# Kernel tuning notes

Hardware: AMD Instinct MI355X
Metric: run time of the kernel (lower is better)

## Reference

```python
import jax, jax.numpy as jnp
import numpy as np

B, S, D, NH = 2, 1024, 2048, 8
QK, V, I = 1024, 2048, 8192  # qk_dim = D/2, v_dim = D, intermediate = 4D
CAP = 15.0
EPS = 1e-6


def setup_inputs() -> dict:
    key = jax.random.key(0)
    ks = jax.random.split(key, 12)
    sc = D ** -0.5
    return {
        "x": jax.random.normal(ks[0], (B, S, D), jnp.float32),
        "Wq": jax.random.normal(ks[1], (D, QK), jnp.float32) * sc,
        "Wk": jax.random.normal(ks[2], (D, QK), jnp.float32) * sc,
        "Wv": jax.random.normal(ks[3], (D, V), jnp.float32) * sc,
        "Wo": jax.random.normal(ks[4], (D, V), jnp.float32) * sc,
        "Wi": jax.random.normal(ks[5], (D, NH), jnp.float32) * sc,
        "bi": -10.0 * jnp.ones((NH,), jnp.float32),   # xLSTM input-gate bias init
        "Wf": jax.random.normal(ks[6], (D, NH), jnp.float32) * sc,
        "bf": jnp.linspace(3.0, 6.0, NH, dtype=jnp.float32),  # forget-gate bias init
        "mh_norm_w": jnp.ones((V,), jnp.float32),
        "Wout": jax.random.normal(ks[7], (V, D), jnp.float32) * (V ** -0.5),
        "rms1_w": jnp.ones((D,), jnp.float32),
        "Wgate": jax.random.normal(ks[8], (D, I), jnp.float32) * sc,
        "Wup": jax.random.normal(ks[9], (D, I), jnp.float32) * sc,
        "Wdown": jax.random.normal(ks[10], (I, D), jnp.float32) * (I ** -0.5),
        "rms2_w": jnp.ones((D,), jnp.float32),
    }


def soft_cap(x, cap=CAP):
    return cap * jnp.tanh(x / cap)


def rms_norm(x, w, eps=EPS):
    xf = x.astype(jnp.float32)
    var = jnp.mean(xf * xf, axis=-1, keepdims=True)
    return (w * (xf * jax.lax.rsqrt(var + eps))).astype(x.dtype)


def mlstm_stabilized(q, k, v, i, f):
    # q,k: [B,NH,S,DQK]; v: [B,NH,S,DV]; i,f: [B,NH,S] (soft-capped preacts)
    dqk = q.shape[-1]
    logf = jax.nn.log_sigmoid(f.astype(jnp.float32))
    lfc = jnp.cumsum(logf, axis=-1)                         # [B,NH,S]
    tri = jnp.tril(jnp.ones((S, S), bool))
    # log decay D[t,s] = sum_{j=s+1..t} log sig(f_j) + i_s  (causal)
    logD = jnp.where(tri, lfc[..., :, None] - lfc[..., None, :], -jnp.inf) + i[..., None, :]
    m = jnp.max(logD, axis=-1, keepdims=True)               # [B,NH,S,1] stabilizer
    Dm = jnp.exp(logD - m)
    scores = jnp.einsum("bhsd,bhtd->bhst", q, k) * (dqk ** -0.5) * Dm
    n = jnp.maximum(jnp.abs(scores.sum(-1, keepdims=True)), jnp.exp(-m))
    return jnp.einsum("bhst,bhtv->bhsv", scores, v) / (n + EPS)  # [B,NH,S,DV]


def xlstm_layer(x, Wq, Wk, Wv, Wo, Wi, bi, Wf, bf, mh_norm_w, Wout):
    q = (x @ Wq).reshape(B, S, NH, -1).transpose(0, 2, 1, 3)
    k = (x @ Wk).reshape(B, S, NH, -1).transpose(0, 2, 1, 3)
    v = (x @ Wv).reshape(B, S, NH, -1).transpose(0, 2, 1, 3)
    o_preact = x @ Wo                                       # [B,S,V]
    i = soft_cap(x @ Wi + bi).transpose(0, 2, 1)            # [B,NH,S]
    f = soft_cap(x @ Wf + bf).transpose(0, 2, 1)
    h = mlstm_stabilized(q, k, v, i, f)                     # [B,NH,S,DV]
    h = h.transpose(0, 2, 1, 3)                             # [B,S,NH,DV]
    # multi-head RMS norm over per-head value dim
    hf = h.astype(jnp.float32)
    var = jnp.mean(hf * hf, axis=-1, keepdims=True)
    hn = (hf * jax.lax.rsqrt(var + EPS)).reshape(B, S, V) * mh_norm_w
    h_out = jax.nn.sigmoid(o_preact) * hn                   # output gate
    return h_out @ Wout


def reference(x, Wq, Wk, Wv, Wo, Wi, bi, Wf, bf, mh_norm_w, Wout, rms1_w,
              Wgate, Wup, Wdown, rms2_w):
    residual = x
    h = xlstm_layer(x, Wq, Wk, Wv, Wo, Wi, bi, Wf, bf, mh_norm_w, Wout)
    h = residual + rms_norm(h, rms1_w)
    mlp = (jax.nn.silu(h @ Wgate) * (h @ Wup)) @ Wdown
    return h + rms_norm(mlp, rms2_w)
```

## Files before the change

kernel.cpp:

```cpp
#include <hip/hip_runtime.h>
#include <hip/hip_bf16.h>

#define TOKENS 2048
#define DMODEL 2048
#define SEQ    1024
#define QKVO   6144

typedef __attribute__((ext_vector_type(8))) short bf16x8;
typedef __attribute__((ext_vector_type(4))) short bf16x4;
typedef __attribute__((ext_vector_type(4))) float f32x4;
typedef __attribute__((ext_vector_type(8))) unsigned short u16x8;
typedef __attribute__((ext_vector_type(4))) unsigned short u16x4;

__device__ __forceinline__ float sigmoidf_(float x) { return 1.f / (1.f + expf(-x)); }
__device__ __forceinline__ float softcapf_(float x) { return 15.f * tanhf(x * (1.f / 15.f)); }
__device__ __forceinline__ float logsigf_(float x) {
  return (x >= 0.f) ? -log1pf(expf(-x)) : (x - log1pf(expf(x)));
}
__device__ __forceinline__ unsigned short f2bf(float f) {
  unsigned u = __builtin_bit_cast(unsigned, f);
  u += 0x7FFFu + ((u >> 16) & 1u);
  return (unsigned short)(u >> 16);
}
__device__ __forceinline__ float bf2f(unsigned short b) {
  unsigned u = ((unsigned)b) << 16;
  return __builtin_bit_cast(float, u);
}

typedef __attribute__((address_space(3))) void lds_void;
typedef const __attribute__((address_space(1))) void gmem_void;
__device__ __forceinline__ void gload16(const void* g, void* l) {
  __builtin_amdgcn_global_load_lds((gmem_void*)g, (lds_void*)l, 16, 0, 0);
}
__device__ __forceinline__ unsigned lds_off(const void* p) {
  return (unsigned)(size_t)(__attribute__((address_space(3))) const void*)p;
}

#if defined(__has_builtin)
#if __has_builtin(__builtin_amdgcn_mfma_f32_16x16x16bf16_1k)
#define HAVE_MFMA16 1
#endif
#endif

__device__ __forceinline__ f32x4 mfma16_bf16(bf16x4 a, bf16x4 b, f32x4 c) {
#ifdef HAVE_MFMA16
  return __builtin_amdgcn_mfma_f32_16x16x16bf16_1k(a, b, c, 0, 0, 0);
#else
  f32x4 d;
  asm volatile("v_mfma_f32_16x16x16_bf16 %0, %1, %2, %3"
               : "=v"(d) : "v"(a), "v"(b), "v"(c));
  return d;
#endif
}

__device__ __forceinline__ bf16x4 tr_read(unsigned addr) {
  bf16x4 d;
  asm volatile("ds_read_b64_tr_b16 %0, %1" : "=v"(d) : "v"(addr));
  return d;
}

__device__ __forceinline__ void remap_block(int& bm, int& bn) {
  const int nbx = gridDim.x, nby = gridDim.y;
  const int bid = blockIdx.y * nbx + blockIdx.x;
  const int q = (nbx * nby) >> 3;
  const int lid = (bid & 7) * q + (bid >> 3);
  bm = lid % nby;
  bn = lid / nby;
}

template <int EPI>
__global__ __launch_bounds__(512) void gemm256(
    const unsigned short* __restrict__ A, const unsigned short* __restrict__ BT,
    void* __restrict__ Cout, const unsigned short* __restrict__ aux,
    int M, int N, int K, int ldk) {
  __shared__ unsigned short lds[3][2][8192];
  const int tid = threadIdx.x;
  int bm, bn;
  remap_block(bm, bn);
  const int m0 = bm * 256, n0 = bn * 256;
  const int wid = tid >> 6, lane = tid & 63;
  const int wr = wid >> 2, wc = wid & 3;
  const int fr = lane & 15, fq = lane >> 4;
  const size_t kz = (size_t)blockIdx.z * K;

  const f32x4 zero = {0.f, 0.f, 0.f, 0.f};
  f32x4 acc[8][4];
#pragma unroll
  for (int m = 0; m < 8; ++m)
#pragma unroll
    for (int n = 0; n < 4; ++n) acc[m][n] = zero;

  const int sr = tid >> 2;
  const int sc = tid & 3;
  const int sgc = sc ^ ((sr + (sr >> 2)) & 3);
  const unsigned short* Asrc = A + kz + (size_t)(m0 + sr) * ldk + sgc * 8;
  const unsigned short* Bsrc = BT + kz + (size_t)(n0 + sr) * ldk + sgc * 8;
  const size_t hstep = (size_t)128 * ldk;
  const int ldst = sr * 32 + sc * 8;

  const int rsw = (fq ^ ((fr + (fr >> 2)) & 3)) * 8;
  const int arow0 = wr * 128 + fr;
  const int brow0 = wc * 64 + fr;

  auto stage = [&](int t) {
    const size_t ko = (size_t)t * 32;
    const int bs = t % 3;
    gload16(Asrc + ko, &lds[bs][0][ldst]);
    gload16(Asrc + ko + hstep, &lds[bs][0][4096 + ldst]);
    gload16(Bsrc + ko, &lds[bs][1][ldst]);
    gload16(Bsrc + ko + hstep, &lds[bs][1][4096 + ldst]);
  };

  const int NT = K >> 5;
  stage(0);
  stage(1);

  for (int t = 0; t < NT; ++t) {
    if (t + 1 < NT) {
      asm volatile("s_waitcnt vmcnt(4)" ::: "memory");
    } else {
      asm volatile("s_waitcnt vmcnt(0)" ::: "memory");
    }
    __builtin_amdgcn_s_barrier();
    if (t + 2 < NT) stage(t + 2);
    const int b = t % 3;
    const unsigned short* la = &lds[b][0][0];
    const unsigned short* lb = &lds[b][1][0];
    bf16x8 bfm[4], af[4];
#pragma unroll
    for (int n = 0; n < 4; ++n)
      bfm[n] = *(const bf16x8*)&lb[(brow0 + n * 16) * 32 + rsw];
#pragma unroll
    for (int m = 0; m < 4; ++m)
      af[m] = *(const bf16x8*)&la[(arow0 + m * 16) * 32 + rsw];
    __builtin_amdgcn_s_setprio(1);
#pragma unroll
    for (int m = 0; m < 4; ++m)
#pragma unroll
      for (int n = 0; n < 4; ++n)
        acc[m][n] = __builtin_amdgcn_mfma_f32_16x16x32_bf16(af[m], bfm[n],
                                                            acc[m][n], 0, 0, 0);
    __builtin_amdgcn_s_setprio(0);
#pragma unroll
    for (int m = 0; m < 4; ++m)
      af[m] = *(const bf16x8*)&la[(arow0 + 64 + m * 16) * 32 + rsw];
    __builtin_amdgcn_s_setprio(1);
#pragma unroll
    for (int m = 0; m < 4; ++m)
#pragma unroll
      for (int n = 0; n < 4; ++n)
        acc[4 + m][n] = __builtin_amdgcn_mfma_f32_16x16x32_bf16(
            af[m], bfm[n], acc[4 + m][n], 0, 0, 0);
    __builtin_amdgcn_s_setprio(0);
  }

  const int orow = m0 + wr * 128 + fq * 4;
  const int ocol = n0 + wc * 64 + fr;
#pragma unroll
  for (int m = 0; m < 8; ++m) {
#pragma unroll
    for (int n = 0; n < 4; ++n) {
      const int cc = ocol + n * 16;
#pragma unroll
      for (int j = 0; j < 4; ++j) {
        const int r = orow + m * 16 + j;
        float v = acc[m][n][j];
        if (EPI == 0) {
          ((float*)Cout + (size_t)blockIdx.z * M * N)[(size_t)r * N + cc] = v;
        } else if (EPI == 1) {
          ((unsigned short*)Cout)[(size_t)r * N + cc] = f2bf(v);
        } else {
          const size_t idx = (size_t)r * N + cc;
          const float gv = bf2f(aux[idx]);
          ((unsigned short*)Cout)[idx] = f2bf(v * gv * sigmoidf_(gv));
        }
      }
    }
  }
}

template <int EPI>
__global__ __launch_bounds__(256) void gemm_bf16(
    const unsigned short* __restrict__ A, const unsigned short* __restrict__ BT,
    void* __restrict__ Cout, int M, int N, int K) {
  __shared__ unsigned short As[2][128 * 32];
  __shared__ unsigned short Bs[2][128 * 32];
  const int tid = threadIdx.x;
  int bm, bn;
  remap_block(bm, bn);
  const int m0 = bm * 128;
  const int n0 = bn * 128;
  const int wid = tid >> 6;
  const int lane = tid & 63;
  const int wr = wid >> 1, wc = wid & 1;
  const int fr = lane & 15, fq = lane >> 4;

  const f32x4 zero = {0.f, 0.f, 0.f, 0.f};
  f32x4 acc[4][4];
#pragma unroll
  for (int m = 0; m < 4; ++m)
#pragma unroll
    for (int n = 0; n < 4; ++n) acc[m][n] = zero;

  const int srow = tid >> 2;
  const int sc = tid & 3;
  const int sgc = sc ^ ((srow + (srow >> 2)) & 3);
  const int scol = sgc * 8;
  const unsigned short* Ag0 = A + (size_t)(m0 + srow) * K + scol;
  const unsigned short* Ag1 = A + (size_t)(m0 + 64 + srow) * K + scol;
  const unsigned short* Bg0 = BT + (size_t)(n0 + srow) * K + scol;
  const unsigned short* Bg1 = BT + (size_t)(n0 + 64 + srow) * K + scol;
  const int rsw = (fq ^ ((fr + (fr >> 2)) & 3)) * 8;

  gload16(Ag0, &As[0][tid * 8]);
  gload16(Ag1, &As[0][2048 + tid * 8]);
  gload16(Bg0, &Bs[0][tid * 8]);
  gload16(Bg1, &Bs[0][2048 + tid * 8]);
  __syncthreads();

  const int nt = K >> 5;
  for (int t = 0; t < nt; ++t) {
    const int cur = t & 1;
    if (t + 1 < nt) {
      const int k0 = (t + 1) << 5;
      gload16(Ag0 + k0, &As[cur ^ 1][tid * 8]);
      gload16(Ag1 + k0, &As[cur ^ 1][2048 + tid * 8]);
      gload16(Bg0 + k0, &Bs[cur ^ 1][tid * 8]);
      gload16(Bg1 + k0, &Bs[cur ^ 1][2048 + tid * 8]);
    }
    bf16x8 af[4], bfm[4];
#pragma unroll
    for (int m = 0; m < 4; ++m)
      af[m] = *(const bf16x8*)&As[cur][(wr * 64 + m * 16 + fr) * 32 + rsw];
#pragma unroll
    for (int n = 0; n < 4; ++n)
      bfm[n] = *(const bf16x8*)&Bs[cur][(wc * 64 + n * 16 + fr) * 32 + rsw];
    __builtin_amdgcn_s_setprio(1);
#pragma unroll
    for (int m = 0; m < 4; ++m)
#pragma unroll
      for (int n = 0; n < 4; ++n)
        acc[m][n] = __builtin_amdgcn_mfma_f32_16x16x32_bf16(af[m], bfm[n],
                                                            acc[m][n], 0, 0, 0);
    __builtin_amdgcn_s_setprio(0);
    __syncthreads();
  }

  const int orow = m0 + wr * 64 + fq * 4;
  const int ocol = n0 + wc * 64 + fr;
#pragma unroll
  for (int m = 0; m < 4; ++m) {
#pragma unroll
    for (int n = 0; n < 4; ++n) {
      const int cc = ocol + n * 16;
#pragma unroll
      for (int j = 0; j < 4; ++j) {
        const int r = orow + m * 16 + j;
        float v = acc[m][n][j];
        if (EPI == 0) ((float*)Cout)[(size_t)r * N + cc] = v;
        else ((unsigned short*)Cout)[(size_t)r * N + cc] = f2bf(v);
      }
    }
  }
}

__global__ __launch_bounds__(256) void castf2b_kernel(
    const float* __restrict__ in, unsigned short* __restrict__ outp) {
  const size_t i = ((size_t)blockIdx.x * 256 + threadIdx.x) * 8;
  float4 a = *(const float4*)&in[i];
  float4 b = *(const float4*)&in[i + 4];
  u16x8 o;
  o[0] = f2bf(a.x); o[1] = f2bf(a.y); o[2] = f2bf(a.z); o[3] = f2bf(a.w);
  o[4] = f2bf(b.x); o[5] = f2bf(b.y); o[6] = f2bf(b.z); o[7] = f2bf(b.w);
  *(u16x8*)&outp[i] = o;
}

__global__ __launch_bounds__(256) void castT_kernel(
    const float* __restrict__ W, unsigned short* __restrict__ WT, int K, int N) {
  __shared__ float tile[128][65];
  const int n0 = blockIdx.x * 64, k0 = blockIdx.y * 128;
  const int rr = threadIdx.x >> 4;
  const int c4 = (threadIdx.x & 15) * 4;
#pragma unroll
  for (int p = 0; p < 8; ++p) {
    const int r = p * 16 + rr;
    float4 v = *(const float4*)&W[(size_t)(k0 + r) * N + n0 + c4];
    tile[r][c4 + 0] = v.x; tile[r][c4 + 1] = v.y;
    tile[r][c4 + 2] = v.z; tile[r][c4 + 3] = v.w;
  }
  __syncthreads();
  const int kc = (threadIdx.x & 15) * 8;
#pragma unroll
  for (int p = 0; p < 4; ++p) {
    const int n = p * 16 + rr;
    u16x8 o;
#pragma unroll
    for (int j = 0; j < 8; ++j) o[j] = f2bf(tile[kc + j][n]);
    *(u16x8*)&WT[(size_t)(n0 + n) * K + k0 + kc] = o;
  }
}

__global__ __launch_bounds__(256) void gatesT_kernel(
    const float* __restrict__ Wi, const float* __restrict__ Wf,
    float* __restrict__ WT) {
  const int idx = blockIdx.x * 256 + threadIdx.x;
  const int row = idx >> 11;
  const int d = idx & 2047;
  const float* W = (row < 8) ? Wi : Wf;
  WT[idx] = W[d * 8 + (row & 7)];
}

__global__ __launch_bounds__(256) void gates_kernel(
    const float* __restrict__ x, const float* __restrict__ WT,
    const float* __restrict__ bi, const float* __restrict__ bf,
    float* __restrict__ icap, float* __restrict__ fls) {
  const int t = blockIdx.x;
  const int tid = threadIdx.x;
  __shared__ float xs[2048];
  *(float4*)&xs[tid * 4] = *(const float4*)&x[(size_t)t * 2048 + tid * 4];
  *(float4*)&xs[1024 + tid * 4] =
      *(const float4*)&x[(size_t)t * 2048 + 1024 + tid * 4];
  __syncthreads();
  const int wave = tid >> 6, lane = tid & 63;
  const int b = t >> 10, s = t & 1023;
  for (int gg = wave; gg < 16; gg += 4) {
    const int head = gg & 7;
    const int isF = gg >> 3;
    const float* Wrow = WT + (size_t)gg * 2048;
    float acc = 0.f;
#pragma unroll
    for (int it = 0; it < 8; ++it) {
      const float4 w4 = *(const float4*)&Wrow[it * 256 + lane * 4];
      const float4 x4 = *(const float4*)&xs[it * 256 + lane * 4];
      acc = fmaf(x4.x, w4.x, acc);
      acc = fmaf(x4.y, w4.y, acc);
      acc = fmaf(x4.z, w4.z, acc);
      acc = fmaf(x4.w, w4.w, acc);
    }
#pragma unroll
    for (int m = 32; m > 0; m >>= 1) acc += __shfl_down(acc, m, 64);
    if (lane == 0) {
      const size_t o = (size_t)(b * 8 + head) * 1024 + s;
      if (isF) fls[o] = logsigf_(softcapf_(acc + bf[head]));
      else icap[o] = softcapf_(acc + bi[head]);
    }
  }
}

__global__ __launch_bounds__(1024) void scan_kernel(
    const float* __restrict__ icap, const float* __restrict__ fls,
    float* __restrict__ lfc, float* __restrict__ garr, float* __restrict__ mx) {
  const int bh = blockIdx.x;
  const int tid = threadIdx.x;
  __shared__ float sm[1024];
  sm[tid] = fls[(size_t)bh * 1024 + tid];
  __syncthreads();
  for (int off = 1; off < 1024; off <<= 1) {
    float v = sm[tid];
    if (tid >= off) v += sm[tid - off];
    __syncthreads();
    sm[tid] = v;
    __syncthreads();
  }
  const float l = sm[tid];
  lfc[(size_t)bh * 1024 + tid] = l;
  const float g = icap[(size_t)bh * 1024 + tid] - l;
  garr[(size_t)bh * 1024 + tid] = g;
  __syncthreads();
  sm[tid] = g;
  __syncthreads();
  for (int off = 1; off < 1024; off <<= 1) {
    float v = sm[tid];
    if (tid >= off) v = fmaxf(v, sm[tid - off]);
    __syncthreads();
    sm[tid] = v;
    __syncthreads();
  }
  mx[(size_t)bh * 1024 + tid] = sm[tid];
}

__global__ __launch_bounds__(128) void mlstm_mfma_kernel(
    const unsigned short* __restrict__ qkvob,
    const float* __restrict__ garr, const float* __restrict__ lfc,
    const float* __restrict__ mx, float* __restrict__ h) {
  __shared__ unsigned short k_lds[32 * 128];
  __shared__ unsigned short v_lds[32 * 256];
  const int tid = threadIdx.x;
  const int lane = tid & 63;
  const int w = tid >> 6;
  const int bh = blockIdx.y;
  const int b = bh >> 3, hh = bh & 7;
  const int tb = blockIdx.x;
  const int fr = lane & 15, fq = lane >> 4;
  const int tw = tb * 32 + w * 16 + fr;
  const size_t tokT = (size_t)(b * SEQ + tw);
  const float scale = 0.08838834764831845f;

  bf16x8 qf[4];
#pragma unroll
  for (int kd = 0; kd < 4; ++kd)
    qf[kd] = *(const bf16x8*)&qkvob[tokT * QKVO + hh * 128 + kd * 32 + fq * 8];

  const float Mt = mx[(size_t)bh * SEQ + tw];
  const float mt = lfc[(size_t)bh * SEQ + tw] + Mt;

  f32x4 acc[16];
  const f32x4 zero = {0.f, 0.f, 0.f, 0.f};
#pragma unroll
  for (int D = 0; D < 16; ++D) acc[D] = zero;
  float asum = 0.f;

  const unsigned vbase = lds_off(v_lds);
  const int nsb = tb + 1;

  for (int sb = 0; sb < nsb; ++sb) {
    const int s0 = sb * 32;
    if (sb) __syncthreads();
#pragma unroll
    for (int it = 0; it < 4; ++it) {
      const int ck = it * 128 + tid;
      const int s = ck >> 4, c = ck & 15;
      const int cg = c ^ (s & 7);
      gload16(&qkvob[(size_t)(b * SEQ + s0 + s) * QKVO + 1024 + hh * 128 + cg * 8],
              &k_lds[ck * 8]);
    }
#pragma unroll
    for (int it = 0; it < 8; ++it) {
      const int cv = it * 128 + tid;
      const int W_ = cv >> 9, D = (cv >> 5) & 15, g = (cv >> 3) & 3,
                jj = (cv >> 1) & 3, c2 = cv & 1;
      const int s = W_ * 16 + g * 4 + jj;
      gload16(&qkvob[(size_t)(b * SEQ + s0 + s) * QKVO + 2048 + hh * 256 +
                     D * 16 + c2 * 8],
              &v_lds[cv * 8]);
    }
    __syncthreads();

#pragma unroll
    for (int st = 0; st < 2; ++st) {
      f32x4 cfrag = zero;
      const int srow = st * 16 + fr;
#pragma unroll
      for (int kd = 0; kd < 4; ++kd) {
        const int cc = (kd * 4 + fq) ^ (srow & 7);
        const bf16x8 kf = *(const bf16x8*)&k_lds[srow * 128 + cc * 8];
        cfrag = __builtin_amdgcn_mfma_f32_16x16x32_bf16(kf, qf[kd], cfrag, 0, 0, 0);
      }
      const int sbase = s0 + st * 16 + fq * 4;
      const float4 g4 = *(const float4*)&garr[(size_t)bh * SEQ + sbase];
      float wv[4];
      wv[0] = (sbase + 0 <= tw) ? cfrag[0] * scale * __expf(g4.x - Mt) : 0.f;
      wv[1] = (sbase + 1 <= tw) ? cfrag[1] * scale * __expf(g4.y - Mt) : 0.f;
      wv[2] = (sbase + 2 <= tw) ? cfrag[2] * scale * __expf(g4.z - Mt) : 0.f;
      wv[3] = (sbase + 3 <= tw) ? cfrag[3] * scale * __expf(g4.w - Mt) : 0.f;
      asum += wv[0] + wv[1] + wv[2] + wv[3];
      bf16x4 pf;
      pf[0] = (short)f2bf(wv[0]); pf[1] = (short)f2bf(wv[1]);
      pf[2] = (short)f2bf(wv[2]); pf[3] = (short)f2bf(wv[3]);

#pragma unroll
      for (int Dg = 0; Dg < 2; ++Dg) {
        bf16x4 vf[8];
#pragma unroll
        for (int D = 0; D < 8; ++D)
          vf[D] = tr_read(vbase + (st * 4096 + (Dg * 8 + D) * 256) * 2 + lane * 8);
        asm volatile("s_waitcnt lgkmcnt(0)" ::: "memory");
        __builtin_amdgcn_sched_barrier(0);
#pragma unroll
        for (int D = 0; D < 8; ++D)
          acc[Dg * 8 + D] = mfma16_bf16(vf[D], pf, acc[Dg * 8 + D]);
      }
    }
  }

  asum += __shfl_xor(asum, 16, 64);
  asum += __shfl_xor(asum, 32, 64);
  const float n = fmaxf(fabsf(asum), __expf(-mt));
  const float inv = 1.f / (n + 1e-6f);
  asm volatile("s_nop 7\n\ts_nop 7" ::);
  float* hrow = &h[tokT * 2048 + hh * 256];
#pragma unroll
  for (int D = 0; D < 16; ++D) {
    float4 o4;
    o4.x = acc[D][0] * inv;
    o4.y = acc[D][1] * inv;
    o4.z = acc[D][2] * inv;
    o4.w = acc[D][3] * inv;
    *(float4*)&hrow[D * 16 + fq * 4] = o4;
  }
}

__global__ __launch_bounds__(256) void hout_kernel(
    const float* __restrict__ h, const unsigned short* __restrict__ qkvob,
    const float* __restrict__ mhw, unsigned short* __restrict__ houtb) {
  const int t = blockIdx.x;
  const int tid = threadIdx.x;
  const size_t base = (size_t)t * 2048 + tid * 8;
  float vals[8];
  *(float4*)&vals[0] = *(const float4*)&h[base];
  *(float4*)&vals[4] = *(const float4*)&h[base + 4];
  float ss = 0.f;
#pragma unroll
  for (int j = 0; j < 8; ++j) ss += vals[j] * vals[j];
#pragma unroll
  for (int m = 16; m > 0; m >>= 1) ss += __shfl_xor(ss, m, 32);
  const float rinv = rsqrtf(ss * (1.f / 256.f) + 1e-6f);
  const u16x8 ovb = *(const u16x8*)&qkvob[(size_t)t * QKVO + 4096 + tid * 8];
  u16x8 res;
#pragma unroll
  for (int j = 0; j < 8; ++j) {
    const float hn = vals[j] * rinv * mhw[tid * 8 + j];
    res[j] = f2bf(hn * sigmoidf_(bf2f(ovb[j])));
  }
  *(u16x8*)&houtb[base] = res;
}

template <int EMIT_BF16, int NY>
__global__ __launch_bounds__(256) void addrms_kernel(
    const float* __restrict__ base_, const float* __restrict__ y0,
    const float* __restrict__ y1, const float* __restrict__ y2,
    const float* __restrict__ y3, const float* __restrict__ w,
    float* __restrict__ outp, unsigned short* __restrict__ outb) {
  const int t = blockIdx.x;
  const int tid = threadIdx.x;
  __shared__ float red[4];
  const size_t boff = (size_t)t * 2048 + tid * 8;
  float vals[8];
  *(float4*)&vals[0] = *(const float4*)&y0[boff];
  *(float4*)&vals[4] = *(const float4*)&y0[boff + 4];
  if (NY == 4) {
    float v1[8];
    *(float4*)&v1[0] = *(const float4*)&y1[boff];
    *(float4*)&v1[4] = *(const float4*)&y1[boff + 4];
#pragma unroll
    for (int j = 0; j < 8; ++j) vals[j] += v1[j];
    *(float4*)&v1[0] = *(const float4*)&y2[boff];
    *(float4*)&v1[4] = *(const float4*)&y2[boff + 4];
#pragma unroll
    for (int j = 0; j < 8; ++j) vals[j] += v1[j];
    *(float4*)&v1[0] = *(const float4*)&y3[boff];
    *(float4*)&v1[4] = *(const float4*)&y3[boff + 4];
#pragma unroll
    for (int j = 0; j < 8; ++j) vals[j] += v1[j];
  }
  float ss = 0.f;
#pragma unroll
  for (int j = 0; j < 8; ++j) ss += vals[j] * vals[j];
#pragma unroll
  for (int m = 32; m > 0; m >>= 1) ss += __shfl_xor(ss, m, 64);
  if ((tid & 63) == 0) red[tid >> 6] = ss;
  __syncthreads();
  ss = red[0] + red[1] + red[2] + red[3];
  const float rinv = rsqrtf(ss * (1.f / 2048.f) + 1e-6f);
  float bv[8];
  *(float4*)&bv[0] = *(const float4*)&base_[boff];
  *(float4*)&bv[4] = *(const float4*)&base_[boff + 4];
  float res[8];
  u16x8 rb;
#pragma unroll
  for (int j = 0; j < 8; ++j) {
    res[j] = bv[j] + vals[j] * rinv * w[tid * 8 + j];
    if (EMIT_BF16) rb[j] = f2bf(res[j]);
  }
  *(float4*)&outp[boff] = *(float4*)&res[0];
  *(float4*)&outp[boff + 4] = *(float4*)&res[4];
  if (EMIT_BF16) *(u16x8*)&outb[boff] = rb;
}

extern "C" void kernel_launch(void* const* d_in, const int* in_sizes, int n_in,
                              void* d_out, int out_size, void* d_ws,
                              size_t ws_size, hipStream_t stream) {
  const float* x = (const float*)d_in[0];
  const float* Wq = (const float*)d_in[1];
  const float* Wk = (const float*)d_in[2];
  const float* Wv = (const float*)d_in[3];
  const float* Wo = (const float*)d_in[4];
  const float* Wi = (const float*)d_in[5];
  const float* bi = (const float*)d_in[6];
  const float* Wf = (const float*)d_in[7];
  const float* bf = (const float*)d_in[8];
  const float* mhw = (const float*)d_in[9];
  const float* Wout = (const float*)d_in[10];
  const float* rms1 = (const float*)d_in[11];
  const float* Wgate = (const float*)d_in[12];
  const float* Wup = (const float*)d_in[13];
  const float* Wdown = (const float*)d_in[14];
  const float* rms2 = (const float*)d_in[15];
  float* out = (float*)d_out;
  char* base = (char*)d_ws;
  const size_t MBy = 1024 * 1024;

  unsigned short* W = (unsigned short*)(base);
  unsigned short* actb = (unsigned short*)(base + 32 * MBy);
  float* gs = (float*)(base + 48 * MBy);
  unsigned short* houtb = (unsigned short*)(base + 48 * MBy);
  float* h = (float*)(base + 64 * MBy);
  float* f1 = (float*)(base + 64 * MBy);
  unsigned short* gbuf = (unsigned short*)(base + 80 * MBy);
  float* mlp = (float*)(base + 80 * MBy);
  unsigned short* xb = (unsigned short*)(base + 112 * MBy);
  unsigned short* f1b = (unsigned short*)(base + 112 * MBy);
  unsigned short* qkvob = (unsigned short*)(base + 120 * MBy);
  float* attn = (float*)(base + 120 * MBy);
  float* icap = gs;
  float* fls = gs + 16384;
  float* lfc = gs + 32768;
  float* garr = gs + 49152;
  float* mxp = gs + 65536;
  float* gwT = gs + 81920;

  const dim3 blk(256);

  castf2b_kernel<<<TOKENS, blk, 0, stream>>>(x, xb);
  gatesT_kernel<<<128, blk, 0, stream>>>(Wi, Wf, gwT);
  gates_kernel<<<TOKENS, blk, 0, stream>>>(x, gwT, bi, bf, icap, fls);
  scan_kernel<<<16, 1024, 0, stream>>>(icap, fls, lfc, garr, mxp);

  castT_kernel<<<dim3(16, 16), blk, 0, stream>>>(Wq, W, 2048, 1024);
  castT_kernel<<<dim3(16, 16), blk, 0, stream>>>(Wk, W + (size_t)1024 * 2048,
                                                 2048, 1024);
  castT_kernel<<<dim3(32, 16), blk, 0, stream>>>(Wv, W + (size_t)2048 * 2048,
                                                 2048, 2048);
  castT_kernel<<<dim3(32, 16), blk, 0, stream>>>(Wo, W + (size_t)4096 * 2048,
                                                 2048, 2048);
  gemm256<1><<<dim3(24, 8), dim3(512), 0, stream>>>(
      xb, W, qkvob, nullptr, TOKENS, 6144, 2048, 2048);

  mlstm_mfma_kernel<<<dim3(32, 16), dim3(128), 0, stream>>>(qkvob, garr, lfc,
                                                            mxp, h);
  hout_kernel<<<TOKENS, blk, 0, stream>>>(h, qkvob, mhw, houtb);

  castT_kernel<<<dim3(32, 16), blk, 0, stream>>>(Wout, W, 2048, 2048);
  gemm_bf16<0><<<dim3(16, 16), blk, 0, stream>>>(houtb, W, attn, TOKENS, 2048,
                                                 2048);

  addrms_kernel<1, 1><<<TOKENS, blk, 0, stream>>>(
      x, attn, nullptr, nullptr, nullptr, rms1, f1, f1b);

  castT_kernel<<<dim3(128, 16), blk, 0, stream>>>(Wgate, W, 2048, 8192);
  gemm256<1><<<dim3(32, 8), dim3(512), 0, stream>>>(
      f1b, W, gbuf, nullptr, TOKENS, 8192, 2048, 2048);
  castT_kernel<<<dim3(128, 16), blk, 0, stream>>>(Wup, W, 2048, 8192);
  gemm256<2><<<dim3(32, 8), dim3(512), 0, stream>>>(
      f1b, W, actb, gbuf, TOKENS, 8192, 2048, 2048);

  castT_kernel<<<dim3(32, 64), blk, 0, stream>>>(Wdown, W, 8192, 2048);
  gemm256<0><<<dim3(8, 8, 4), dim3(512), 0, stream>>>(
      actb, W, mlp, nullptr, TOKENS, 2048, 2048, 8192);

  addrms_kernel<0, 4><<<TOKENS, blk, 0, stream>>>(
      f1, mlp, mlp + 4194304, mlp + 8388608, mlp + 12582912, rms2, out,
      nullptr);
}
```

Baseline: 521.9 us.

## Load GEMM B fragments directly to registers and fuse x cast into gates

The 256x256 GEMM now stages only the A tile through double-buffered LDS. Each wave loads its B fragments straight from global memory into registers, one step ahead, instead of triple-buffering both operands in LDS. This cuts LDS traffic and footprint, but replaces vmcnt-based pipelining with a full __syncthreads per step and uses uncoalesced per-lane global loads for B, which waves sharing a column block will fetch redundantly. Separately, the standalone fp32-to-bf16 cast of x is folded into the gates kernel, which already holds x in shared memory, removing one launch and one read of x.

```diff
diff --git a/kernel.cpp b/kernel.cpp
--- a/kernel.cpp
+++ b/kernel.cpp
@@ -73,7 +73,7 @@
     const unsigned short* __restrict__ A, const unsigned short* __restrict__ BT,
     void* __restrict__ Cout, const unsigned short* __restrict__ aux,
     int M, int N, int K, int ldk) {
-  __shared__ unsigned short lds[3][2][8192];
+  __shared__ unsigned short As[2][8192];
   const int tid = threadIdx.x;
   int bm, bn;
   remap_block(bm, bn);
@@ -94,64 +94,74 @@
   const int sc = tid & 3;
   const int sgc = sc ^ ((sr + (sr >> 2)) & 3);
   const unsigned short* Asrc = A + kz + (size_t)(m0 + sr) * ldk + sgc * 8;
-  const unsigned short* Bsrc = BT + kz + (size_t)(n0 + sr) * ldk + sgc * 8;
   const size_t hstep = (size_t)128 * ldk;
   const int ldst = sr * 32 + sc * 8;
 
+  auto stageA = [&](int t) {
+    const size_t ko = (size_t)t * 32;
+    unsigned short* d = &As[t & 1][ldst];
+    gload16(Asrc + ko, d);
+    gload16(Asrc + ko + hstep, d + 4096);
+  };
+
+  const unsigned short* Bp0 = BT + kz + (size_t)(n0 + wc * 64 + 0 * 16 + fr) * ldk + fq * 8;
+  const unsigned short* Bp1 = BT + kz + (size_t)(n0 + wc * 64 + 1 * 16 + fr) * ldk + fq * 8;
+  const unsigned short* Bp2 = BT + kz + (size_t)(n0 + wc * 64 + 2 * 16 + fr) * ldk + fq * 8;
+  const unsigned short* Bp3 = BT + kz + (size_t)(n0 + wc * 64 + 3 * 16 + fr) * ldk + fq * 8;
+
   const int rsw = (fq ^ ((fr + (fr >> 2)) & 3)) * 8;
-  const int arow0 = wr * 128 + fr;
-  const int brow0 = wc * 64 + fr;
-
-  auto stage = [&](int t) {
+  const int aoff = (wr * 128 + fr) * 32 + rsw;
+
+  bf16x8 bf0[4], bf1[4];
+  auto loadB = [&](int t, bf16x8* dst) {
     const size_t ko = (size_t)t * 32;
-    const int bs = t % 3;
-    gload16(Asrc + ko, &lds[bs][0][ldst]);
-    gload16(Asrc + ko + hstep, &lds[bs][0][4096 + ldst]);
-    gload16(Bsrc + ko, &lds[bs][1][ldst]);
-    gload16(Bsrc + ko + hstep, &lds[bs][1][4096 + ldst]);
+    dst[0] = *(const bf16x8*)(Bp0 + ko);
+    dst[1] = *(const bf16x8*)(Bp1 + ko);
+    dst[2] = *(const bf16x8*)(Bp2 + ko);
+    dst[3] = *(const bf16x8*)(Bp3 + ko);
   };
 
-  const int NT = K >> 5;
-  stage(0);
-  stage(1);
-
-  for (int t = 0; t < NT; ++t) {
-    if (t + 1 < NT) {
-      asm volatile("s_waitcnt vmcnt(4)" ::: "memory");
-    } else {
-      asm volatile("s_waitcnt vmcnt(0)" ::: "memory");
-    }
-    __builtin_amdgcn_s_barrier();
-    if (t + 2 < NT) stage(t + 2);
-    const int b = t % 3;
-    const unsigned short* la = &lds[b][0][0];
-    const unsigned short* lb = &lds[b][1][0];
-    bf16x8 bfm[4], af[4];
-#pragma unroll
-    for (int n = 0; n < 4; ++n)
-      bfm[n] = *(const bf16x8*)&lb[(brow0 + n * 16) * 32 + rsw];
+  auto body = [&](int t, bf16x8* bcur, bf16x8* bnext) {
+    const int NTl = K >> 5;
+    if (t + 1 < NTl) {
+      loadB(t + 1, bnext);
+      stageA(t + 1);
+    }
+    const unsigned short* la = &As[t & 1][0];
+    bf16x8 af[4];
 #pragma unroll
     for (int m = 0; m < 4; ++m)
-      af[m] = *(const bf16x8*)&la[(arow0 + m * 16) * 32 + rsw];
+      af[m] = *(const bf16x8*)&la[aoff + m * 512];
     __builtin_amdgcn_s_setprio(1);
 #pragma unroll
     for (int m = 0; m < 4; ++m)
 #pragma unroll
       for (int n = 0; n < 4; ++n)
-        acc[m][n] = __builtin_amdgcn_mfma_f32_16x16x32_bf16(af[m], bfm[n],
+        acc[m][n] = __builtin_amdgcn_mfma_f32_16x16x32_bf16(af[m], bcur[n],
                                                             acc[m][n], 0, 0, 0);
     __builtin_amdgcn_s_setprio(0);
 #pragma unroll
     for (int m = 0; m < 4; ++m)
-      af[m] = *(const bf16x8*)&la[(arow0 + 64 + m * 16) * 32 + rsw];
+      af[m] = *(const bf16x8*)&la[aoff + (64 * 32) + m * 512];
     __builtin_amdgcn_s_setprio(1);
 #pragma unroll
     for (int m = 0; m < 4; ++m)
 #pragma unroll
       for (int n = 0; n < 4; ++n)
         acc[4 + m][n] = __builtin_amdgcn_mfma_f32_16x16x32_bf16(
-            af[m], bfm[n], acc[4 + m][n], 0, 0, 0);
+            af[m], bcur[n], acc[4 + m][n], 0, 0, 0);
     __builtin_amdgcn_s_setprio(0);
+    __syncthreads();
+  };
+
+  const int NT = K >> 5;
+  loadB(0, bf0);
+  stageA(0);
+  __syncthreads();
+
+  for (int t = 0; t < NT; t += 2) {
+    body(t, bf0, bf1);
+    body(t + 1, bf1, bf0);
   }
 
   const int orow = m0 + wr * 128 + fq * 4;
@@ -264,17 +274,6 @@
   }
 }
 
-__global__ __launch_bounds__(256) void castf2b_kernel(
-    const float* __restrict__ in, unsigned short* __restrict__ outp) {
-  const size_t i = ((size_t)blockIdx.x * 256 + threadIdx.x) * 8;
-  float4 a = *(const float4*)&in[i];
-  float4 b = *(const float4*)&in[i + 4];
-  u16x8 o;
-  o[0] = f2bf(a.x); o[1] = f2bf(a.y); o[2] = f2bf(a.z); o[3] = f2bf(a.w);
-  o[4] = f2bf(b.x); o[5] = f2bf(b.y); o[6] = f2bf(b.z); o[7] = f2bf(b.w);
-  *(u16x8*)&outp[i] = o;
-}
-
 __global__ __launch_bounds__(256) void castT_kernel(
     const float* __restrict__ W, unsigned short* __restrict__ WT, int K, int N) {
   __shared__ float tile[128][65];
@@ -313,7 +312,8 @@
 __global__ __launch_bounds__(256) void gates_kernel(
     const float* __restrict__ x, const float* __restrict__ WT,
     const float* __restrict__ bi, const float* __restrict__ bf,
-    float* __restrict__ icap, float* __restrict__ fls) {
+    float* __restrict__ icap, float* __restrict__ fls,
+    unsigned short* __restrict__ xb) {
   const int t = blockIdx.x;
   const int tid = threadIdx.x;
   __shared__ float xs[2048];
@@ -321,6 +321,12 @@
   *(float4*)&xs[1024 + tid * 4] =
       *(const float4*)&x[(size_t)t * 2048 + 1024 + tid * 4];
   __syncthreads();
+  {
+    u16x8 o;
+#pragma unroll
+    for (int j = 0; j < 8; ++j) o[j] = f2bf(xs[tid * 8 + j]);
+    *(u16x8*)&xb[(size_t)t * 2048 + tid * 8] = o;
+  }
   const int wave = tid >> 6, lane = tid & 63;
   const int b = t >> 10, s = t & 1023;
   for (int gg = wave; gg < 16; gg += 4) {
@@ -611,9 +617,8 @@
 
   const dim3 blk(256);
 
-  castf2b_kernel<<<TOKENS, blk, 0, stream>>>(x, xb);
   gatesT_kernel<<<128, blk, 0, stream>>>(Wi, Wf, gwT);
-  gates_kernel<<<TOKENS, blk, 0, stream>>>(x, gwT, bi, bf, icap, fls);
+  gates_kernel<<<TOKENS, blk, 0, stream>>>(x, gwT, bi, bf, icap, fls, xb);
   scan_kernel<<<16, 1024, 0, stream>>>(icap, fls, lfc, garr, mxp);
 
   castT_kernel<<<dim3(16, 16), blk, 0, stream>>>(Wq, W, 2048, 1024);
```

Measured after the change: 651.9 us. +24.9%, slower.
